# Kernel optimization log

Hardware: AMD Instinct MI355X
Metric: run time of the kernel (lower is better)

## Reference

```python
import math
import jax, jax.numpy as jnp
import numpy as np

R, C, D, ORDER = 2048, 2048, 64, 3
O = ORDER + 1  # var_size


def setup_inputs() -> dict:
    key = jax.random.key(0)
    k1, k2, k3, k4, k5, k6 = jax.random.split(key, 6)
    return {
        "events": jax.random.randint(k1, (R, C), 0, 2, dtype=jnp.int32),
        "col_times": jax.random.uniform(k2, (C,), dtype=jnp.float32),
        "z_rows": jax.random.normal(k3, (O, R, D), dtype=jnp.float32),
        "z_cols": jax.random.normal(k4, (C, D), dtype=jnp.float32),
        "gamma_rows": jax.random.uniform(k5, (R,), dtype=jnp.float32),
        "gamma_cols": jax.random.uniform(k6, (C,), dtype=jnp.float32),
    }


def reference(events, col_times, z_rows, z_cols, gamma_rows, gamma_cols):
    o = z_rows.shape[0]
    facts = np.array([math.factorial(i) for i in range(o)], dtype=np.float32)
    # Taylor time-basis: coeffs[o, c] = t_c^o / o!   (replaces nested Python loops)
    coeffs = jnp.stack([col_times ** i for i in range(o)]) / facts[:, None]  # (O, C)
    # row positions at each column's time: (R, C, D)
    pos = jnp.einsum('ord,oc->rcd', z_rows, coeffs)
    diff = pos - z_cols[None, :, :]                        # (R, C, D)
    dist = jnp.sqrt(jnp.sum(diff * diff, axis=-1))         # (R, C) pairwise L2
    logit = gamma_rows[:, None] + gamma_cols[None, :] - dist
    # log p where p = 1 - E - (1-2E)*sigmoid(logit):
    #   E==1 -> log sigmoid(logit); E==0 -> log sigmoid(-logit)
    sign = jnp.where(events == 1, 1.0, -1.0).astype(logit.dtype)
    log_lik = jnp.sum(jax.nn.log_sigmoid(sign * logit))
    return -log_lik
```

## Files before the change

kernel.cpp:

```cpp
#include <hip/hip_runtime.h>
#include <hip/hip_bf16.h>
#include <math.h>

#define R_DIM 2048
#define C_DIM 2048
#define D_DIM 64
#define O_DIM 4
#define K_USED 272
#define K_TOT 288
#define WB_WORDS (C_DIM / 64)

typedef __attribute__((ext_vector_type(8))) short short8;
typedef __attribute__((ext_vector_type(4))) float floatx4;


__device__ __forceinline__ ushort f2bf(float f) {
  unsigned u = __float_as_uint(f);
  return (ushort)((u + 0x7FFFu + ((u >> 16) & 1u)) >> 16);
}

__device__ __forceinline__ void load16_lds(const void* g, void* l) {
  auto gp = reinterpret_cast<const __attribute__((address_space(1))) unsigned int*>(
      reinterpret_cast<uintptr_t>(g));
  auto lp = reinterpret_cast<__attribute__((address_space(3))) unsigned int*>(
      (unsigned int)reinterpret_cast<uintptr_t>(l));
  __builtin_amdgcn_global_load_lds(gp, lp, 16, 0, 0);
}

__global__ void prep_kernel(const int* __restrict__ events,
                            const float* __restrict__ col_times,
                            const float* __restrict__ z_rows,
                            const float* __restrict__ z_cols,
                            ushort* __restrict__ Ab,
                            ushort* __restrict__ Bb,
                            float* __restrict__ nzc,
                            unsigned long long* __restrict__ Wb,
                            float* __restrict__ out) {
  const int b = blockIdx.x;
  const int t = threadIdx.x;
  const int w = t >> 6;
  const int lane = t & 63;

  if (b == 0 && t == 0) out[0] = 0.0f;

  if (b < 512) {
    const int r = b * 4 + w;
    float zv[O_DIM];
#pragma unroll
    for (int o = 0; o < O_DIM; ++o) {
      zv[o] = z_rows[(size_t)(o * R_DIM + r) * D_DIM + lane];
      Ab[(size_t)r * K_TOT + o * 64 + lane] = f2bf(zv[o]);
    }
    float g00 = zv[0] * zv[0], g01 = zv[0] * zv[1], g02 = zv[0] * zv[2],
          g03 = zv[0] * zv[3], g11 = zv[1] * zv[1], g12 = zv[1] * zv[2],
          g13 = zv[1] * zv[3], g22 = zv[2] * zv[2], g23 = zv[2] * zv[3],
          g33 = zv[3] * zv[3];
#pragma unroll
    for (int off = 32; off > 0; off >>= 1) {
      g00 += __shfl_xor(g00, off); g01 += __shfl_xor(g01, off);
      g02 += __shfl_xor(g02, off); g03 += __shfl_xor(g03, off);
      g11 += __shfl_xor(g11, off); g12 += __shfl_xor(g12, off);
      g13 += __shfl_xor(g13, off); g22 += __shfl_xor(g22, off);
      g23 += __shfl_xor(g23, off); g33 += __shfl_xor(g33, off);
    }
    if (lane == 0) {
      ushort* e = Ab + (size_t)r * K_TOT + 256;
      e[0] = f2bf(g00);  e[1] = f2bf(g01);  e[2] = f2bf(g02);  e[3] = f2bf(g03);
      e[4] = f2bf(g01);  e[5] = f2bf(g11);  e[6] = f2bf(g12);  e[7] = f2bf(g13);
      e[8] = f2bf(g02);  e[9] = f2bf(g12);  e[10] = f2bf(g22); e[11] = f2bf(g23);
      e[12] = f2bf(g03); e[13] = f2bf(g13); e[14] = f2bf(g23); e[15] = f2bf(g33);
    }
    if (lane < 16) Ab[(size_t)r * K_TOT + K_USED + lane] = 0;
  } else if (b < 1024) {
    const int c = (b - 512) * 4 + w;
    const float tt = col_times[c];
    float cf[4];
    cf[0] = 1.0f; cf[1] = tt; cf[2] = tt * tt * 0.5f;
    cf[3] = tt * tt * tt * (1.0f / 6.0f);
    const float zc = z_cols[(size_t)c * D_DIM + lane];
#pragma unroll
    for (int o = 0; o < O_DIM; ++o)
      Bb[(size_t)c * K_TOT + o * 64 + lane] = f2bf(-2.0f * cf[o] * zc);
    float q = zc * zc;
#pragma unroll
    for (int off = 32; off > 0; off >>= 1) q += __shfl_xor(q, off);
    if (lane == 0) {
      nzc[c] = q;
      ushort* e = Bb + (size_t)c * K_TOT + 256;
#pragma unroll
      for (int i = 0; i < 16; ++i) e[i] = f2bf(cf[i >> 2] * cf[i & 3]);
    }
    if (lane < 16) Bb[(size_t)c * K_TOT + K_USED + lane] = 0;
  } else {
    const int r = b - 1024;
    const int cbase = w * 512;
#pragma unroll
    for (int i = 0; i < 8; ++i) {
      const int col = cbase + i * 64 + lane;
      const int ev = events[(size_t)r * C_DIM + col];
      const unsigned long long mask = __ballot(ev == 1);
      if (lane == 0) Wb[r * WB_WORDS + (cbase >> 6) + i] = mask;
    }
  }
}

__launch_bounds__(256, 4)
__global__ void pair_kernel(const float* __restrict__ gamma_rows,
                            const float* __restrict__ gamma_cols,
                            const ushort* __restrict__ Ab,
                            const ushort* __restrict__ Bb,
                            const float* __restrict__ nzc,
                            const unsigned long long* __restrict__ Wb,
                            float* __restrict__ out) {
  __shared__ __align__(16) ushort As[64 * 32];
  __shared__ __align__(16) ushort Bs[64 * 32];
  __shared__ float red[4];

  const int t = threadIdx.x;
  const int widx = t >> 6;
  const int lane = t & 63;
  const int m0 = blockIdx.y * 64;
  const int c0 = blockIdx.x * 64;
  const int wm = widx & 1;
  const int wn = widx >> 1;
  const int lm = lane & 15;
  const int kg = lane >> 4;

  floatx4 acc[2][2];
#pragma unroll
  for (int i = 0; i < 2; ++i)
#pragma unroll
    for (int j = 0; j < 2; ++j) acc[i][j] = (floatx4){0.f, 0.f, 0.f, 0.f};

  const int srow = t >> 2;
  const int selem = (t & 3) * 8;

  for (int kt = 0; kt < K_TOT; kt += 32) {
    load16_lds(Ab + (size_t)(m0 + srow) * K_TOT + kt + selem,
               (char*)As + widx * 1024);
    load16_lds(Bb + (size_t)(c0 + srow) * K_TOT + kt + selem,
               (char*)Bs + widx * 1024);
    __syncthreads();

    short8 a[2], b[2];
#pragma unroll
    for (int mt = 0; mt < 2; ++mt)
      a[mt] = *(const short8*)(As + (wm * 32 + mt * 16 + lm) * 32 + kg * 8);
#pragma unroll
    for (int nt = 0; nt < 2; ++nt)
      b[nt] = *(const short8*)(Bs + (wn * 32 + nt * 16 + lm) * 32 + kg * 8);
#pragma unroll
    for (int mt = 0; mt < 2; ++mt)
#pragma unroll
      for (int nt = 0; nt < 2; ++nt)
        acc[mt][nt] = __builtin_amdgcn_mfma_f32_16x16x32_bf16(
            a[mt], b[nt], acc[mt][nt], 0, 0, 0);
    __syncthreads();
  }

  float gc[2], nz[2];
  int cbit[2];
#pragma unroll
  for (int nt = 0; nt < 2; ++nt) {
    const int c = c0 + wn * 32 + nt * 16 + lm;
    gc[nt] = gamma_cols[c];
    nz[nt] = nzc[c];
    cbit[nt] = c & 63;
  }
  const int wword = blockIdx.x;
  float lsum = 0.0f;
#pragma unroll
  for (int mt = 0; mt < 2; ++mt) {
    const int rbase = m0 + wm * 32 + mt * 16 + kg * 4;
#pragma unroll
    for (int j = 0; j < 4; ++j) {
      const int r = rbase + j;
      const float gr = gamma_rows[r];
      const unsigned long long wbits = Wb[r * WB_WORDS + wword];
#pragma unroll
      for (int nt = 0; nt < 2; ++nt) {
        const float d2 = acc[mt][nt][j] + nz[nt];
        const float dist = sqrtf(fmaxf(d2, 0.0f));
        const float logit = gr + gc[nt] - dist;
        const int ev = (int)((wbits >> cbit[nt]) & 1ull);
        const float x = ev ? -logit : logit;
        lsum += fmaxf(x, 0.0f) + __logf(1.0f + __expf(-fabsf(x)));
      }
    }
  }
#pragma unroll
  for (int off = 32; off > 0; off >>= 1) lsum += __shfl_down(lsum, off);
  if (lane == 0) red[widx] = lsum;
  __syncthreads();
  if (t == 0) atomicAdd(out, red[0] + red[1] + red[2] + red[3]);
}

extern "C" void kernel_launch(void* const* d_in, const int* in_sizes, int n_in,
                              void* d_out, int out_size, void* d_ws, size_t ws_size,
                              hipStream_t stream) {
  const int* events = (const int*)d_in[0];
  const float* col_times = (const float*)d_in[1];
  const float* z_rows = (const float*)d_in[2];
  const float* z_cols = (const float*)d_in[3];
  const float* gamma_rows = (const float*)d_in[4];
  const float* gamma_cols = (const float*)d_in[5];
  float* out = (float*)d_out;

  ushort* Ab = (ushort*)d_ws;
  ushort* Bb = Ab + (size_t)R_DIM * K_TOT;
  float* nzc = (float*)(Bb + (size_t)C_DIM * K_TOT);
  unsigned long long* Wb = (unsigned long long*)(nzc + C_DIM);

  prep_kernel<<<3072, 256, 0, stream>>>(events, col_times, z_rows, z_cols, Ab,
                                        Bb, nzc, Wb, out);
  dim3 grid(C_DIM / 64, R_DIM / 64);
  pair_kernel<<<grid, 256, 0, stream>>>(gamma_rows, gamma_cols, Ab, Bb, nzc, Wb,
                                        out);
}
```

Before: 95.49 us.

## Fuse prep and pairwise kernels with in-block bf16 operand construction

Removes the separate prep kernel: each block loads its fp32 z_rows/z_cols tile, converts it to bf16, and builds the Gram and Taylor cross terms directly in LDS. The MFMA runs in two phases over LDS, with orders 0-1 first and then orders 2-3 plus the Gram terms. Events are read directly instead of through a precomputed bitmask. The final reduction switches from a float atomicAdd to a last-block reduction over per-block partials. Each block recomputes row and column operands redundantly (32x per row tile), and the events reads become scattered int32 loads.

```diff
diff --git a/kernel.cpp b/kernel.cpp
--- a/kernel.cpp
+++ b/kernel.cpp
@@ -5,169 +5,174 @@
 #define R_DIM 2048
 #define C_DIM 2048
 #define D_DIM 64
-#define O_DIM 4
-#define K_USED 272
-#define K_TOT 288
-#define WB_WORDS (C_DIM / 64)
+#define KSTRIDE 168
 
 typedef __attribute__((ext_vector_type(8))) short short8;
 typedef __attribute__((ext_vector_type(4))) float floatx4;
-
 
 __device__ __forceinline__ ushort f2bf(float f) {
   unsigned u = __float_as_uint(f);
   return (ushort)((u + 0x7FFFu + ((u >> 16) & 1u)) >> 16);
 }
-
-__device__ __forceinline__ void load16_lds(const void* g, void* l) {
-  auto gp = reinterpret_cast<const __attribute__((address_space(1))) unsigned int*>(
-      reinterpret_cast<uintptr_t>(g));
-  auto lp = reinterpret_cast<__attribute__((address_space(3))) unsigned int*>(
-      (unsigned int)reinterpret_cast<uintptr_t>(l));
-  __builtin_amdgcn_global_load_lds(gp, lp, 16, 0, 0);
-}
-
-__global__ void prep_kernel(const int* __restrict__ events,
-                            const float* __restrict__ col_times,
-                            const float* __restrict__ z_rows,
-                            const float* __restrict__ z_cols,
-                            ushort* __restrict__ Ab,
-                            ushort* __restrict__ Bb,
-                            float* __restrict__ nzc,
-                            unsigned long long* __restrict__ Wb,
-                            float* __restrict__ out) {
-  const int b = blockIdx.x;
+__device__ __forceinline__ ushort4 pack4(float4 v) {
+  ushort4 r;
+  r.x = f2bf(v.x); r.y = f2bf(v.y); r.z = f2bf(v.z); r.w = f2bf(v.w);
+  return r;
+}
+__device__ __forceinline__ float4 scale4(float s, float4 v) {
+  float4 r;
+  r.x = s * v.x; r.y = s * v.y; r.z = s * v.z; r.w = s * v.w;
+  return r;
+}
+__device__ __forceinline__ float dot4(float4 a, float4 b) {
+  return fmaf(a.x, b.x, fmaf(a.y, b.y, fmaf(a.z, b.z, a.w * b.w)));
+}
+
+__launch_bounds__(256, 3)
+__global__ void fused_kernel(const int* __restrict__ events,
+                             const float* __restrict__ col_times,
+                             const float* __restrict__ z_rows,
+                             const float* __restrict__ z_cols,
+                             const float* __restrict__ gamma_rows,
+                             const float* __restrict__ gamma_cols,
+                             unsigned* __restrict__ cnt,
+                             float* __restrict__ parts,
+                             float* __restrict__ out) {
+  __shared__ __align__(16) ushort As[64 * KSTRIDE];
+  __shared__ __align__(16) ushort Bs[64 * KSTRIDE];
+  __shared__ float nzc_s[64];
+  __shared__ float red[4];
+  __shared__ float flag;
+
   const int t = threadIdx.x;
-  const int w = t >> 6;
-  const int lane = t & 63;
-
-  if (b == 0 && t == 0) out[0] = 0.0f;
-
-  if (b < 512) {
-    const int r = b * 4 + w;
-    float zv[O_DIM];
-#pragma unroll
-    for (int o = 0; o < O_DIM; ++o) {
-      zv[o] = z_rows[(size_t)(o * R_DIM + r) * D_DIM + lane];
-      Ab[(size_t)r * K_TOT + o * 64 + lane] = f2bf(zv[o]);
+  const int widx = t >> 6, lane = t & 63;
+  const int m0 = blockIdx.y * 64, c0 = blockIdx.x * 64;
+  const int wm = widx & 1, wn = widx >> 1;
+  const int lm = lane & 15, kg = lane >> 4;
+
+  const int rr = t >> 2;
+  const int ch = t & 3;
+  const int d0 = ch * 16;
+
+  float4 av[4][4];
+#pragma unroll
+  for (int o = 0; o < 4; ++o)
+#pragma unroll
+    for (int i = 0; i < 4; ++i)
+      av[o][i] = *(const float4*)&z_rows[(size_t)(o * R_DIM + m0 + rr) * D_DIM + d0 + i * 4];
+  float4 bv[4];
+#pragma unroll
+  for (int i = 0; i < 4; ++i)
+    bv[i] = *(const float4*)&z_cols[(size_t)(c0 + rr) * D_DIM + d0 + i * 4];
+  const float tt = col_times[c0 + rr];
+  float cf[4];
+  cf[0] = 1.0f; cf[1] = tt; cf[2] = tt * tt * 0.5f; cf[3] = cf[2] * tt * (1.0f / 3.0f);
+
+#pragma unroll
+  for (int o = 0; o < 2; ++o) {
+    const float s = -2.0f * cf[o];
+#pragma unroll
+    for (int i = 0; i < 4; ++i) {
+      *(ushort4*)&As[rr * KSTRIDE + o * 64 + d0 + i * 4] = pack4(av[o][i]);
+      *(ushort4*)&Bs[rr * KSTRIDE + o * 64 + d0 + i * 4] = pack4(scale4(s, bv[i]));
     }
-    float g00 = zv[0] * zv[0], g01 = zv[0] * zv[1], g02 = zv[0] * zv[2],
-          g03 = zv[0] * zv[3], g11 = zv[1] * zv[1], g12 = zv[1] * zv[2],
-          g13 = zv[1] * zv[3], g22 = zv[2] * zv[2], g23 = zv[2] * zv[3],
-          g33 = zv[3] * zv[3];
-#pragma unroll
-    for (int off = 32; off > 0; off >>= 1) {
-      g00 += __shfl_xor(g00, off); g01 += __shfl_xor(g01, off);
-      g02 += __shfl_xor(g02, off); g03 += __shfl_xor(g03, off);
-      g11 += __shfl_xor(g11, off); g12 += __shfl_xor(g12, off);
-      g13 += __shfl_xor(g13, off); g22 += __shfl_xor(g22, off);
-      g23 += __shfl_xor(g23, off); g33 += __shfl_xor(g33, off);
+  }
+  float q = dot4(bv[0], bv[0]) + dot4(bv[1], bv[1]) + dot4(bv[2], bv[2]) + dot4(bv[3], bv[3]);
+  q += __shfl_xor(q, 1); q += __shfl_xor(q, 2);
+  if (ch == 0) nzc_s[rr] = q;
+
+  __syncthreads();
+
+  floatx4 acc[2][2];
+#pragma unroll
+  for (int i = 0; i < 2; ++i)
+#pragma unroll
+    for (int j = 0; j < 2; ++j) acc[i][j] = (floatx4){0.f, 0.f, 0.f, 0.f};
+
+#pragma unroll
+  for (int kt = 0; kt < 128; kt += 32) {
+    short8 a[2], b[2];
+#pragma unroll
+    for (int mt = 0; mt < 2; ++mt)
+      a[mt] = *(const short8*)&As[(wm * 32 + mt * 16 + lm) * KSTRIDE + kt + kg * 8];
+#pragma unroll
+    for (int nt = 0; nt < 2; ++nt)
+      b[nt] = *(const short8*)&Bs[(wn * 32 + nt * 16 + lm) * KSTRIDE + kt + kg * 8];
+#pragma unroll
+    for (int mt = 0; mt < 2; ++mt)
+#pragma unroll
+      for (int nt = 0; nt < 2; ++nt)
+        acc[mt][nt] = __builtin_amdgcn_mfma_f32_16x16x32_bf16(a[mt], b[nt], acc[mt][nt], 0, 0, 0);
+  }
+
+  __syncthreads();
+
+#pragma unroll
+  for (int o = 2; o < 4; ++o) {
+    const float s = -2.0f * cf[o];
+#pragma unroll
+    for (int i = 0; i < 4; ++i) {
+      *(ushort4*)&As[rr * KSTRIDE + (o - 2) * 64 + d0 + i * 4] = pack4(av[o][i]);
+      *(ushort4*)&Bs[rr * KSTRIDE + (o - 2) * 64 + d0 + i * 4] = pack4(scale4(s, bv[i]));
     }
-    if (lane == 0) {
-      ushort* e = Ab + (size_t)r * K_TOT + 256;
-      e[0] = f2bf(g00);  e[1] = f2bf(g01);  e[2] = f2bf(g02);  e[3] = f2bf(g03);
-      e[4] = f2bf(g01);  e[5] = f2bf(g11);  e[6] = f2bf(g12);  e[7] = f2bf(g13);
-      e[8] = f2bf(g02);  e[9] = f2bf(g12);  e[10] = f2bf(g22); e[11] = f2bf(g23);
-      e[12] = f2bf(g03); e[13] = f2bf(g13); e[14] = f2bf(g23); e[15] = f2bf(g33);
-    }
-    if (lane < 16) Ab[(size_t)r * K_TOT + K_USED + lane] = 0;
-  } else if (b < 1024) {
-    const int c = (b - 512) * 4 + w;
-    const float tt = col_times[c];
-    float cf[4];
-    cf[0] = 1.0f; cf[1] = tt; cf[2] = tt * tt * 0.5f;
-    cf[3] = tt * tt * tt * (1.0f / 6.0f);
-    const float zc = z_cols[(size_t)c * D_DIM + lane];
-#pragma unroll
-    for (int o = 0; o < O_DIM; ++o)
-      Bb[(size_t)c * K_TOT + o * 64 + lane] = f2bf(-2.0f * cf[o] * zc);
-    float q = zc * zc;
-#pragma unroll
-    for (int off = 32; off > 0; off >>= 1) q += __shfl_xor(q, off);
-    if (lane == 0) {
-      nzc[c] = q;
-      ushort* e = Bb + (size_t)c * K_TOT + 256;
-#pragma unroll
-      for (int i = 0; i < 16; ++i) e[i] = f2bf(cf[i >> 2] * cf[i & 3]);
-    }
-    if (lane < 16) Bb[(size_t)c * K_TOT + K_USED + lane] = 0;
-  } else {
-    const int r = b - 1024;
-    const int cbase = w * 512;
-#pragma unroll
-    for (int i = 0; i < 8; ++i) {
-      const int col = cbase + i * 64 + lane;
-      const int ev = events[(size_t)r * C_DIM + col];
-      const unsigned long long mask = __ballot(ev == 1);
-      if (lane == 0) Wb[r * WB_WORDS + (cbase >> 6) + i] = mask;
-    }
-  }
-}
-
-__launch_bounds__(256, 4)
-__global__ void pair_kernel(const float* __restrict__ gamma_rows,
-                            const float* __restrict__ gamma_cols,
-                            const ushort* __restrict__ Ab,
-                            const ushort* __restrict__ Bb,
-                            const float* __restrict__ nzc,
-                            const unsigned long long* __restrict__ Wb,
-                            float* __restrict__ out) {
-  __shared__ __align__(16) ushort As[64 * 32];
-  __shared__ __align__(16) ushort Bs[64 * 32];
-  __shared__ float red[4];
-
-  const int t = threadIdx.x;
-  const int widx = t >> 6;
-  const int lane = t & 63;
-  const int m0 = blockIdx.y * 64;
-  const int c0 = blockIdx.x * 64;
-  const int wm = widx & 1;
-  const int wn = widx >> 1;
-  const int lm = lane & 15;
-  const int kg = lane >> 4;
-
-  floatx4 acc[2][2];
-#pragma unroll
-  for (int i = 0; i < 2; ++i)
-#pragma unroll
-    for (int j = 0; j < 2; ++j) acc[i][j] = (floatx4){0.f, 0.f, 0.f, 0.f};
-
-  const int srow = t >> 2;
-  const int selem = (t & 3) * 8;
-
-  for (int kt = 0; kt < K_TOT; kt += 32) {
-    load16_lds(Ab + (size_t)(m0 + srow) * K_TOT + kt + selem,
-               (char*)As + widx * 1024);
-    load16_lds(Bb + (size_t)(c0 + srow) * K_TOT + kt + selem,
-               (char*)Bs + widx * 1024);
-    __syncthreads();
-
+  }
+  float g[10];
+#pragma unroll
+  for (int p = 0; p < 10; ++p) g[p] = 0.0f;
+#pragma unroll
+  for (int i = 0; i < 4; ++i) {
+    const float4 a0 = av[0][i], a1 = av[1][i], a2 = av[2][i], a3 = av[3][i];
+    g[0] += dot4(a0, a0); g[1] += dot4(a0, a1); g[2] += dot4(a0, a2);
+    g[3] += dot4(a0, a3); g[4] += dot4(a1, a1); g[5] += dot4(a1, a2);
+    g[6] += dot4(a1, a3); g[7] += dot4(a2, a2); g[8] += dot4(a2, a3);
+    g[9] += dot4(a3, a3);
+  }
+#pragma unroll
+  for (int p = 0; p < 10; ++p) {
+    g[p] += __shfl_xor(g[p], 1);
+    g[p] += __shfl_xor(g[p], 2);
+  }
+  if (ch == 0) {
+    ushort* ea = &As[rr * KSTRIDE + 128];
+    ea[0] = f2bf(g[0]); ea[1] = f2bf(g[1]); ea[2] = f2bf(g[2]); ea[3] = f2bf(g[3]);
+    ea[4] = f2bf(g[1]); ea[5] = f2bf(g[4]); ea[6] = f2bf(g[5]); ea[7] = f2bf(g[6]);
+    ea[8] = f2bf(g[2]); ea[9] = f2bf(g[5]); ea[10] = f2bf(g[7]); ea[11] = f2bf(g[8]);
+    ea[12] = f2bf(g[3]); ea[13] = f2bf(g[6]); ea[14] = f2bf(g[8]); ea[15] = f2bf(g[9]);
+#pragma unroll
+    for (int z = 16; z < 32; ++z) ea[z] = 0;
+    ushort* eb = &Bs[rr * KSTRIDE + 128];
+#pragma unroll
+    for (int i = 0; i < 16; ++i) eb[i] = f2bf(cf[i >> 2] * cf[i & 3]);
+#pragma unroll
+    for (int z = 16; z < 32; ++z) eb[z] = 0;
+  }
+  __syncthreads();
+
+#pragma unroll
+  for (int kt = 0; kt < 160; kt += 32) {
     short8 a[2], b[2];
 #pragma unroll
     for (int mt = 0; mt < 2; ++mt)
-      a[mt] = *(const short8*)(As + (wm * 32 + mt * 16 + lm) * 32 + kg * 8);
+      a[mt] = *(const short8*)&As[(wm * 32 + mt * 16 + lm) * KSTRIDE + kt + kg * 8];
 #pragma unroll
     for (int nt = 0; nt < 2; ++nt)
-      b[nt] = *(const short8*)(Bs + (wn * 32 + nt * 16 + lm) * 32 + kg * 8);
+      b[nt] = *(const short8*)&Bs[(wn * 32 + nt * 16 + lm) * KSTRIDE + kt + kg * 8];
 #pragma unroll
     for (int mt = 0; mt < 2; ++mt)
 #pragma unroll
       for (int nt = 0; nt < 2; ++nt)
-        acc[mt][nt] = __builtin_amdgcn_mfma_f32_16x16x32_bf16(
-            a[mt], b[nt], acc[mt][nt], 0, 0, 0);
-    __syncthreads();
+        acc[mt][nt] = __builtin_amdgcn_mfma_f32_16x16x32_bf16(a[mt], b[nt], acc[mt][nt], 0, 0, 0);
   }
 
   float gc[2], nz[2];
-  int cbit[2];
+  int cidx[2];
 #pragma unroll
   for (int nt = 0; nt < 2; ++nt) {
     const int c = c0 + wn * 32 + nt * 16 + lm;
+    cidx[nt] = c;
     gc[nt] = gamma_cols[c];
-    nz[nt] = nzc[c];
-    cbit[nt] = c & 63;
-  }
-  const int wword = blockIdx.x;
+    nz[nt] = nzc_s[c - c0];
+  }
   float lsum = 0.0f;
 #pragma unroll
   for (int mt = 0; mt < 2; ++mt) {
@@ -176,13 +181,12 @@
     for (int j = 0; j < 4; ++j) {
       const int r = rbase + j;
       const float gr = gamma_rows[r];
-      const unsigned long long wbits = Wb[r * WB_WORDS + wword];
 #pragma unroll
       for (int nt = 0; nt < 2; ++nt) {
+        const int ev = events[(size_t)r * C_DIM + cidx[nt]];
         const float d2 = acc[mt][nt][j] + nz[nt];
         const float dist = sqrtf(fmaxf(d2, 0.0f));
         const float logit = gr + gc[nt] - dist;
-        const int ev = (int)((wbits >> cbit[nt]) & 1ull);
         const float x = ev ? -logit : logit;
         lsum += fmaxf(x, 0.0f) + __logf(1.0f + __expf(-fabsf(x)));
       }
@@ -192,7 +196,26 @@
   for (int off = 32; off > 0; off >>= 1) lsum += __shfl_down(lsum, off);
   if (lane == 0) red[widx] = lsum;
   __syncthreads();
-  if (t == 0) atomicAdd(out, red[0] + red[1] + red[2] + red[3]);
+
+  const int bid = blockIdx.y * gridDim.x + blockIdx.x;
+  if (t == 0) {
+    const float bs = red[0] + red[1] + red[2] + red[3];
+    atomicExch(&parts[bid], bs);
+    __threadfence();
+    const unsigned old = atomicAdd(cnt, 1u);
+    flag = (old == 1023u) ? 1.0f : 0.0f;
+  }
+  __syncthreads();
+  if (flag != 0.0f) {
+    __threadfence();
+    float s = 0.0f;
+    for (int i = t; i < 1024; i += 256) s += atomicAdd(&parts[i], 0.0f);
+#pragma unroll
+    for (int off = 32; off > 0; off >>= 1) s += __shfl_down(s, off);
+    if (lane == 0) red[widx] = s;
+    __syncthreads();
+    if (t == 0) out[0] = red[0] + red[1] + red[2] + red[3];
+  }
 }
 
 extern "C" void kernel_launch(void* const* d_in, const int* in_sizes, int n_in,
@@ -204,16 +227,13 @@
   const float* z_cols = (const float*)d_in[3];
   const float* gamma_rows = (const float*)d_in[4];
   const float* gamma_cols = (const float*)d_in[5];
-  float* out = (float*)d_out;
-
-  ushort* Ab = (ushort*)d_ws;
-  ushort* Bb = Ab + (size_t)R_DIM * K_TOT;
-  float* nzc = (float*)(Bb + (size_t)C_DIM * K_TOT);
-  unsigned long long* Wb = (unsigned long long*)(nzc + C_DIM);
-
-  prep_kernel<<<3072, 256, 0, stream>>>(events, col_times, z_rows, z_cols, Ab,
-                                        Bb, nzc, Wb, out);
+
+  unsigned* cnt = (unsigned*)d_ws;
+  float* parts = (float*)d_ws + 16;
+  hipMemsetAsync(d_ws, 0, 4, stream);
+
   dim3 grid(C_DIM / 64, R_DIM / 64);
-  pair_kernel<<<grid, 256, 0, stream>>>(gamma_rows, gamma_cols, Ab, Bb, nzc, Wb,
-                                        out);
-}
+  fused_kernel<<<grid, 256, 0, stream>>>(events, col_times, z_rows, z_cols,
+                                         gamma_rows, gamma_cols, cnt, parts,
+                                         (float*)d_out);
+}
```

New measurement: 109.6 us. 14.8% more time.
